# Kernel tuning notes

Measured on AMD Instinct MI355X. Metric: run time of the kernel, lower is better.

## Reference

```python
import jax, jax.numpy as jnp
import numpy as np

B, S, H, W, T, D = 256, 128, 14, 14, 12, 512


def _lin(key, fan_in, fan_out):
    k1, k2 = jax.random.split(key)
    bound = 1.0 / np.sqrt(fan_in)
    Wm = jax.random.uniform(k1, (fan_in, fan_out), jnp.float32, -bound, bound)
    b = jax.random.uniform(k2, (fan_out,), jnp.float32, -bound, bound)
    return Wm, b


def setup_inputs() -> dict:
    key = jax.random.key(0)
    ks = jax.random.split(key, 20)
    inp = {
        "ci_1": jax.random.normal(ks[0], (B, D), jnp.float32),
        "mi_1": jax.random.normal(ks[1], (B, D), jnp.float32),
        "q": jax.random.normal(ks[2], (B, D), jnp.float32),
        "cws": jax.random.normal(ks[3], (B, S, D), jnp.float32),
        "K": jax.random.normal(ks[4], (B, H, W, D), jnp.float32),
        "C_past": jax.random.normal(ks[5], (B, T, D), jnp.float32),
        "M_past": jax.random.normal(ks[6], (B, T, D), jnp.float32),
    }
    inp["W_cq"], inp["b_cq"] = _lin(ks[7], D, D)          # control_qi
    inp["W_cqi"], inp["b_cqi"] = _lin(ks[8], 2 * D, D)    # cqi_linear
    inp["W_cai"], inp["b_cai"] = _lin(ks[9], D, 1)        # cais_linear
    inp["W_rm"], inp["b_rm"] = _lin(ks[10], D, D)         # memory_read_m
    inp["W_rk"], inp["b_rk"] = _lin(ks[11], D, D)         # memory_read_k
    inp["W_rik"], inp["b_rik"] = _lin(ks[12], 2 * D, D)   # memory_read_ik
    inp["W_rci"], inp["b_rci"] = _lin(ks[13], D, D)       # memory_read_ci_i
    inp["W_wrm"], inp["b_wrm"] = _lin(ks[14], 2 * D, D)   # memory_write_ri_mi_1
    inp["W_wcc"], inp["b_wcc"] = _lin(ks[15], D, 1)       # memory_write_ci_cj
    inp["W_wsa"], inp["b_wsa"] = _lin(ks[16], D, D)       # memory_write_mi_sa
    inp["W_winfo"], inp["b_winfo"] = _lin(ks[17], D, D)   # memory_write_mi_info
    inp["W_wci"], inp["b_wci"] = _lin(ks[18], D, 1)       # memory_write_ci
    return inp


def reference(ci_1, mi_1, q, cws, K, C_past, M_past,
              W_cq, b_cq, W_cqi, b_cqi, W_cai, b_cai,
              W_rm, b_rm, W_rk, b_rk, W_rik, b_rik, W_rci, b_rci,
              W_wrm, b_wrm, W_wcc, b_wcc, W_wsa, b_wsa,
              W_winfo, b_winfo, W_wci, b_wci):
    # ---- control ----
    qi = q @ W_cq + b_cq                                        # [B,D]
    cqi = jnp.concatenate([ci_1, qi], axis=1) @ W_cqi + b_cqi   # [B,D]
    cqi_cws = cqi[:, None, :] * cws                             # [B,S,D]
    cai = cqi_cws @ W_cai + b_cai                               # [B,S,1]
    cvis = jax.nn.softmax(cai, axis=1)
    ci = (cvis * cws).sum(axis=1)                               # [B,D]

    # ---- read ----
    Ii = (mi_1 @ W_rm + b_rm)[:, None, None, :] * (K @ W_rk + b_rk)  # [B,H,W,D]
    Ii_prime = jnp.concatenate([Ii, K], axis=3) @ W_rik + b_rik      # [B,H,W,D]
    rai = (ci[:, None, None, :] * Ii_prime) @ W_rci + b_rci          # [B,H,W,D]
    rvi = jax.nn.softmax(rai, axis=1)   # softmax over H
    rvi = jax.nn.softmax(rvi, axis=2)   # then softmax of those probs over W (faithful)
    ri = (rvi * K).sum(axis=(1, 2))                                  # [B,D]

    # ---- write ----
    mi_info = jnp.concatenate([ri, mi_1], axis=1) @ W_wrm + b_wrm    # [B,D]
    ci_cj = ci[:, None, :] * C_past                                  # [B,T,D]
    saij = jax.nn.softmax(ci_cj @ W_wcc + b_wcc, axis=1)             # [B,T,1]
    mi_sa = (saij * M_past).sum(axis=1)                              # [B,D]
    mi_prime = (mi_sa @ W_wsa + b_wsa) + (mi_info @ W_winfo + b_winfo)
    gate = jax.nn.sigmoid(ci @ W_wci + b_wci)                        # [B,1]
    mi = gate * mi_1 + (1.0 - gate) * mi_prime
    return (ci, mi)
```

## Files before the change

### kernel.cpp

```cpp
#include <hip/hip_runtime.h>
#include <hip/hip_bf16.h>

typedef unsigned short u16;
typedef __attribute__((ext_vector_type(8))) short short8;
typedef __attribute__((ext_vector_type(4))) float f4;

static __device__ __forceinline__ float b2f(u16 u) {
    union { unsigned int i; float f; } x; x.i = ((unsigned int)u) << 16; return x.f;
}
static __device__ __forceinline__ u16 f2b(float f) {
    union { float f; unsigned int i; } x; x.f = f;
    unsigned int r = x.i + 0x7fffu + ((x.i >> 16) & 1u);
    return (u16)(r >> 16);
}
static __device__ __forceinline__ float wave_reduce_sum(float v) {
    #pragma unroll
    for (int off = 32; off > 0; off >>= 1) v += __shfl_down(v, off, 64);
    return v;
}
static __device__ __forceinline__ void gl2lds(const void* g, void* l) {
    __builtin_amdgcn_global_load_lds(
        (const __attribute__((address_space(1))) void*)g,
        (__attribute__((address_space(3))) void*)l, 16, 0, 0);
}

__global__ __launch_bounds__(256) void conv_f32_bf16(
    const float* __restrict__ src, u16* __restrict__ dst, int n)
{
    int i = (blockIdx.x * 256 + threadIdx.x) * 4;
    if (i >= n) return;
    float4 v = *(const float4*)(src + i);
    union { u16 u[4]; uint2 d; } o;
    o.u[0] = f2b(v.x); o.u[1] = f2b(v.y); o.u[2] = f2b(v.z); o.u[3] = f2b(v.w);
    *(uint2*)(dst + i) = o.d;
}

__global__ __launch_bounds__(256) void transpose_k(
    const float* __restrict__ in, u16* __restrict__ out,
    int K, int N, int out_stride, int k_off)
{
    __shared__ float t[32][33];
    int kb = blockIdx.x * 32, nb = blockIdx.y * 32;
    int tx = threadIdx.x, ty = threadIdx.y;
    #pragma unroll
    for (int i = 0; i < 4; i++)
        t[ty + i * 8][tx] = in[(size_t)(kb + ty + i * 8) * N + nb + tx];
    __syncthreads();
    #pragma unroll
    for (int i = 0; i < 4; i++)
        out[(size_t)(nb + ty + i * 8) * out_stride + k_off + kb + tx] =
            f2b(t[tx][ty + i * 8]);
}

template<int MT, int NT>
__global__ __launch_bounds__(256) void gemm_mfma(
    const u16* __restrict__ A0, const u16* __restrict__ A1,
    int M, int K0, int K1, int N,
    const u16* __restrict__ Bt,
    const float* __restrict__ bias0, const float* __restrict__ bias1,
    int epi_mode, const float* __restrict__ E, int m_div,
    const float* __restrict__ gate, const float* __restrict__ mi1,
    void* __restrict__ Cout, int out_f32)
{
    constexpr int BM = MT * 32, BN = NT * 32;
    constexpr int STG = (BM + BN) * 32;
    constexpr int NPF = MT / 2 + NT / 2;
    constexpr int STAGE_B = 3 * STG * 2;
    __shared__ __align__(16) char smem[STAGE_B];
    short* stg = (short*)smem;

    int tid  = threadIdx.x;
    int wave = tid >> 6, lane = tid & 63;
    int wm = wave >> 1, wn = wave & 1;
    int lrow = lane & 15, quad = lane >> 4;

    int gx = gridDim.x, gy = gridDim.y;
    int bx = blockIdx.x, by = blockIdx.y;
    if ((gy & 7) == 0) {
        int lin = by * gx + bx;
        int xcd = lin & 7, j = lin >> 3;
        by = xcd * (gy >> 3) + j / gx;
        bx = j % gx;
    }
    int bm0 = by * BM, bn0 = bx * BN;
    int Ktot = K0 + K1;
    int KT = Ktot >> 5;

    int r16 = lane >> 2, cc = lane & 3;
    int sw = (r16 >> 1) & 3;
    int coff = (cc ^ sw) * 8;

    auto stage = [&](int s, int k0) {
        const u16* asrc; int lda;
        if (k0 < K0) { asrc = A0 + k0; lda = K0; }
        else         { asrc = A1 + (k0 - K0); lda = K1; }
        short* As = stg + s * STG;
        short* Bs = As + BM * 32;
        #pragma unroll
        for (int i = 0; i < MT / 2; i++) {
            int ar = wave * (BM / 4) + 16 * i;
            gl2lds(asrc + (size_t)(bm0 + ar + r16) * lda + coff, As + ar * 32);
        }
        #pragma unroll
        for (int i = 0; i < NT / 2; i++) {
            int br = wave * (BN / 4) + 16 * i;
            gl2lds(Bt + (size_t)(bn0 + br + r16) * Ktot + k0 + coff, Bs + br * 32);
        }
    };

    f4 acc[MT][NT];
    #pragma unroll
    for (int i = 0; i < MT; i++)
        #pragma unroll
        for (int j = 0; j < NT; j++)
            acc[i][j] = (f4){0.f, 0.f, 0.f, 0.f};

    stage(0, 0);
    if (KT > 1) stage(1, 32);
    int sb = 0;
    int sw2 = (lrow >> 1) & 3;
    for (int kt = 0; kt < KT; kt++) {
        if (kt + 1 < KT) {
            if constexpr (NPF == 2)
                asm volatile("s_waitcnt vmcnt(2) lgkmcnt(0)\ns_barrier" ::: "memory");
            else
                asm volatile("s_waitcnt vmcnt(0) lgkmcnt(0)\ns_barrier" ::: "memory");
        } else {
            asm volatile("s_waitcnt vmcnt(0) lgkmcnt(0)\ns_barrier" ::: "memory");
        }
        const short* Ab = stg + sb * STG;
        const short* Bb = Ab + BM * 32;
        if (kt + 2 < KT) {
            int s2 = sb + 2; if (s2 >= 3) s2 -= 3;
            stage(s2, (kt + 2) * 32);
        }
        short8 af[MT], bfr[NT];
        #pragma unroll
        for (int mt = 0; mt < MT; mt++)
            af[mt] = *(const short8*)&Ab[(wm * (MT * 16) + mt * 16 + lrow) * 32 + (quad ^ sw2) * 8];
        #pragma unroll
        for (int nt = 0; nt < NT; nt++)
            bfr[nt] = *(const short8*)&Bb[(wn * (NT * 16) + nt * 16 + lrow) * 32 + (quad ^ sw2) * 8];
        #pragma unroll
        for (int mt = 0; mt < MT; mt++)
            #pragma unroll
            for (int nt = 0; nt < NT; nt++)
                acc[mt][nt] = __builtin_amdgcn_mfma_f32_16x16x32_bf16(
                    af[mt], bfr[nt], acc[mt][nt], 0, 0, 0);
        sb = (sb + 1 == 3) ? 0 : sb + 1;
    }

    #pragma unroll
    for (int nt = 0; nt < NT; nt++) {
        int n = bn0 + wn * (NT * 16) + nt * 16 + lrow;
        float bv = 0.f;
        if (bias0) bv += bias0[n];
        if (bias1) bv += bias1[n];
        #pragma unroll
        for (int mt = 0; mt < MT; mt++) {
            #pragma unroll
            for (int r = 0; r < 4; r++) {
                int m = bm0 + wm * (MT * 16) + mt * 16 + quad * 4 + r;
                float v = acc[mt][nt][r] + bv;
                if (epi_mode == 1) {
                    v *= E[(size_t)(m / m_div) * N + n];
                } else if (epi_mode == 2) {
                    float g = gate[m];
                    v = g * mi1[(size_t)m * N + n] + (1.f - g) * v;
                }
                if (out_f32) ((float*)Cout)[(size_t)m * N + n] = v;
                else         ((u16*)Cout)[(size_t)m * N + n] = f2b(v);
            }
        }
    }
}

__global__ __launch_bounds__(512, 2) void fused_read(
    const u16* __restrict__ kbf, int M,
    const u16* __restrict__ Wrk,  const float* __restrict__ brk,  const float* __restrict__ E1,
    const u16* __restrict__ Wrik, const float* __restrict__ brik, const float* __restrict__ E2,
    const u16* __restrict__ Wrci, const float* __restrict__ brci,
    u16* __restrict__ rai)
{
    __shared__ __align__(16) char smem[139264];
    short* g_tile = (short*)smem;
    short* stgbase = (short*)(smem + 65536);

    int tid = threadIdx.x, wave = tid >> 6, lane = tid & 63;
    int lrow = lane & 15, quad = lane >> 4;
    int r16 = lane >> 2, cc = lane & 3;
    int sw = (r16 >> 1) & 3;
    int coff = (cc ^ sw) * 8;
    int sw2 = (lrow >> 1) & 3;

    int bid = blockIdx.x;
    { int nb = gridDim.x; if ((nb & 7) == 0) { int x = bid & 7, j = bid >> 3; bid = x * (nb >> 3) + j; } }
    int bm0 = bid * 64;

    auto stageB = [&](short* bf, const u16* Wt, int ldk, int k0) {
        short* Bs = bf + 2048;
        #pragma unroll
        for (int i = 0; i < 4; i++) {
            int br = wave * 64 + i * 16;
            gl2lds(Wt + (size_t)(br + r16) * ldk + k0 + coff, Bs + br * 32);
        }
    };
    auto stageA = [&](short* bf, int k0) {
        if (wave < 4) {
            int ar = wave * 16;
            gl2lds(kbf + (size_t)(bm0 + ar + r16) * 512 + k0 + coff, bf + ar * 32);
        }
    };

    f4 acc[4][4];
    auto clr = [&]() {
        #pragma unroll
        for (int t = 0; t < 4; t++)
            #pragma unroll
            for (int nt = 0; nt < 4; nt++)
                acc[t][nt] = (f4){0.f, 0.f, 0.f, 0.f};
    };

    auto kstep = [&](const short* bf, int aMode, int kc0) {
        short8 af[4], bfrag[4];
        #pragma unroll
        for (int t = 0; t < 4; t++) {
            int R = t * 16 + lrow;
            if (aMode == 0)
                af[t] = *(const short8*)&bf[R * 32 + (quad ^ sw2) * 8];
            else {
                int kc = kc0 + quad;
                af[t] = *(const short8*)&g_tile[R * 512 + ((kc ^ (R & 7)) << 3)];
            }
        }
        const short* Bs = bf + 2048;
        #pragma unroll
        for (int nt = 0; nt < 4; nt++)
            bfrag[nt] = *(const short8*)&Bs[(wave * 64 + nt * 16 + lrow) * 32 + (quad ^ sw2) * 8];
        __builtin_amdgcn_s_setprio(1);
        #pragma unroll
        for (int t = 0; t < 4; t++)
            #pragma unroll
            for (int nt = 0; nt < 4; nt++)
                acc[t][nt] = __builtin_amdgcn_mfma_f32_16x16x32_bf16(
                    af[t], bfrag[nt], acc[t][nt], 0, 0, 0);
        __builtin_amdgcn_s_setprio(0);
    };

    int bt0 = bm0 / 196, bt1 = (bm0 + 63) / 196;
    int rsw = (bt1 != bt0) ? (bt1 * 196 - bm0) : 64;
    auto epi_to_gtile = [&](const float* bias, const float* E) {
        #pragma unroll
        for (int nt = 0; nt < 4; nt++) {
            int n = wave * 64 + nt * 16 + lrow;
            float bv = bias[n];
            float e0 = E[(size_t)bt0 * 512 + n];
            float e1 = E[(size_t)bt1 * 512 + n];
            #pragma unroll
            for (int t = 0; t < 4; t++)
                #pragma unroll
                for (int r = 0; r < 4; r++) {
                    int row = t * 16 + quad * 4 + r;
                    float e = (row < rsw) ? e0 : e1;
                    u16 h = f2b((acc[t][nt][r] + bv) * e);
                    int chunk = (n >> 3) ^ (row & 7);
                    g_tile[row * 512 + chunk * 8 + (n & 7)] = (short)h;
                }
        }
    };

    clr();
    stageA(stgbase, 0); stageB(stgbase, Wrk, 512, 0);
    for (int kt = 0; kt < 16; kt++) {
        short* cur = stgbase + (kt & 1) * 18432;
        short* nxt = stgbase + ((kt & 1) ^ 1) * 18432;
        if (kt + 1 < 16) {
            stageA(nxt, (kt + 1) * 32); stageB(nxt, Wrk, 512, (kt + 1) * 32);
            if (wave < 4) asm volatile("s_waitcnt vmcnt(5) lgkmcnt(0)\ns_barrier" ::: "memory");
            else          asm volatile("s_waitcnt vmcnt(4) lgkmcnt(0)\ns_barrier" ::: "memory");
        } else
            asm volatile("s_waitcnt vmcnt(0) lgkmcnt(0)\ns_barrier" ::: "memory");
        kstep(cur, 0, 0);
        asm volatile("s_waitcnt lgkmcnt(0)\ns_barrier" ::: "memory");
    }
    epi_to_gtile(brk, E1);
    __syncthreads();

    clr();
    stageB(stgbase, Wrik, 1024, 0);
    for (int kt = 0; kt < 16; kt++) {
        short* cur = stgbase + (kt & 1) * 18432;
        short* nxt = stgbase + ((kt & 1) ^ 1) * 18432;
        if (kt + 1 < 16) {
            stageB(nxt, Wrik, 1024, (kt + 1) * 32);
            asm volatile("s_waitcnt vmcnt(4) lgkmcnt(0)\ns_barrier" ::: "memory");
        } else
            asm volatile("s_waitcnt vmcnt(0) lgkmcnt(0)\ns_barrier" ::: "memory");
        kstep(cur, 1, kt * 4);
        asm volatile("s_waitcnt lgkmcnt(0)\ns_barrier" ::: "memory");
    }
    stageA(stgbase, 0); stageB(stgbase, Wrik, 1024, 512);
    for (int kt = 0; kt < 16; kt++) {
        short* cur = stgbase + (kt & 1) * 18432;
        short* nxt = stgbase + ((kt & 1) ^ 1) * 18432;
        if (kt + 1 < 16) {
            stageA(nxt, (kt + 1) * 32); stageB(nxt, Wrik, 1024, 512 + (kt + 1) * 32);
            if (wave < 4) asm volatile("s_waitcnt vmcnt(5) lgkmcnt(0)\ns_barrier" ::: "memory");
            else          asm volatile("s_waitcnt vmcnt(4) lgkmcnt(0)\ns_barrier" ::: "memory");
        } else
            asm volatile("s_waitcnt vmcnt(0) lgkmcnt(0)\ns_barrier" ::: "memory");
        kstep(cur, 0, 0);
        asm volatile("s_waitcnt lgkmcnt(0)\ns_barrier" ::: "memory");
    }
    epi_to_gtile(brik, E2);
    __syncthreads();

    clr();
    stageB(stgbase, Wrci, 512, 0);
    for (int kt = 0; kt < 16; kt++) {
        short* cur = stgbase + (kt & 1) * 18432;
        short* nxt = stgbase + ((kt & 1) ^ 1) * 18432;
        if (kt + 1 < 16) {
            stageB(nxt, Wrci, 512, (kt + 1) * 32);
            asm volatile("s_waitcnt vmcnt(4) lgkmcnt(0)\ns_barrier" ::: "memory");
        } else
            asm volatile("s_waitcnt vmcnt(0) lgkmcnt(0)\ns_barrier" ::: "memory");
        kstep(cur, 1, kt * 4);
        asm volatile("s_waitcnt lgkmcnt(0)\ns_barrier" ::: "memory");
    }
    #pragma unroll
    for (int nt = 0; nt < 4; nt++) {
        int n = wave * 64 + nt * 16 + lrow;
        float bv = brci[n];
        #pragma unroll
        for (int t = 0; t < 4; t++)
            #pragma unroll
            for (int r = 0; r < 4; r++) {
                int row = t * 16 + quad * 4 + r;
                g_tile[row * 512 + n] = (short)f2b(acc[t][nt][r] + bv);
            }
    }
    __syncthreads();
    #pragma unroll
    for (int p = 0; p < 8; p++) {
        int idx = p * 512 + tid;
        short8 v = *(const short8*)&g_tile[idx * 8];
        *(short8*)&rai[(size_t)bm0 * 512 + (size_t)idx * 8] = v;
    }
}

__global__ __launch_bounds__(256) void control_attn(
    const float* __restrict__ cqi, const float* __restrict__ cws,
    const float* __restrict__ Wcai, const float* __restrict__ bcai,
    float* __restrict__ ci_f32, float* __restrict__ ci_out)
{
    int b = blockIdx.x, tid = threadIdx.x;
    __shared__ float tW[512];
    __shared__ float p[128];
    __shared__ float inv_l;
    for (int d = tid; d < 512; d += 256)
        tW[d] = cqi[(size_t)b * 512 + d] * Wcai[d];
    __syncthreads();
    int wave = tid >> 6, lane = tid & 63;
    const float* cwsb = cws + (size_t)b * 128 * 512;
    for (int s = wave; s < 128; s += 4) {
        const float* row = cwsb + (size_t)s * 512 + lane * 8;
        float acc = 0.f;
        #pragma unroll
        for (int j = 0; j < 8; j++) acc += tW[lane * 8 + j] * row[j];
        acc = wave_reduce_sum(acc);
        if (lane == 0) p[s] = acc + bcai[0];
    }
    __syncthreads();
    if (tid == 0) {
        float m = -1e30f;
        for (int s = 0; s < 128; s++) m = fmaxf(m, p[s]);
        float l = 0.f;
        for (int s = 0; s < 128; s++) { float e = __expf(p[s] - m); p[s] = e; l += e; }
        inv_l = 1.f / l;
    }
    __syncthreads();
    float inv = inv_l;
    for (int d = tid; d < 512; d += 256) {
        float acc = 0.f;
        for (int s = 0; s < 128; s++) acc += p[s] * cwsb[(size_t)s * 512 + d];
        acc *= inv;
        ci_f32[(size_t)b * 512 + d] = acc;
        ci_out[(size_t)b * 512 + d] = acc;
    }
}

__global__ __launch_bounds__(256) void read_reduce(
    const u16* __restrict__ rai, const u16* __restrict__ Kb, u16* __restrict__ ri)
{
    int b = blockIdx.x >> 1;
    int d = ((blockIdx.x & 1) << 8) + threadIdx.x;
    const u16* rb = rai + (size_t)b * 196 * 512 + d;
    const u16* kb = Kb + (size_t)b * 196 * 512 + d;
    float m1[14], il1[14];
    #pragma unroll
    for (int w = 0; w < 14; w++) {
        float m = -1e30f, s = 0.f;
        #pragma unroll
        for (int h = 0; h < 14; h++) {
            float v = b2f(rb[(size_t)(h * 14 + w) * 512]);
            float nm = fmaxf(m, v);
            s = s * __expf(m - nm) + __expf(v - nm);
            m = nm;
        }
        m1[w] = m; il1[w] = 1.f / s;
    }
    float acc = 0.f;
    #pragma unroll
    for (int h = 0; h < 14; h++) {
        float pv[14], ss = 0.f;
        #pragma unroll
        for (int w = 0; w < 14; w++) {
            float pr = __expf(b2f(rb[(size_t)(h * 14 + w) * 512]) - m1[w]) * il1[w];
            float e = __expf(pr);
            pv[w] = e; ss += e;
        }
        float il2 = 1.f / ss;
        #pragma unroll
        for (int w = 0; w < 14; w++)
            acc += pv[w] * il2 * b2f(kb[(size_t)(h * 14 + w) * 512]);
    }
    ri[(size_t)b * 512 + d] = f2b(acc);
}

__global__ __launch_bounds__(256) void write_attn(
    const float* __restrict__ ci_f32, const float* __restrict__ C_past,
    const float* __restrict__ M_past,
    const float* __restrict__ Wwcc, const float* __restrict__ bwcc,
    const float* __restrict__ Wwci, const float* __restrict__ bwci,
    u16* __restrict__ mi_sa, float* __restrict__ gate)
{
    int b = blockIdx.x, tid = threadIdx.x;
    __shared__ float c[512];
    __shared__ float pt[12];
    __shared__ float red[256];
    for (int d = tid; d < 512; d += 256) c[d] = ci_f32[(size_t)b * 512 + d];
    __syncthreads();
    float g = 0.f;
    for (int d = tid; d < 512; d += 256) g += c[d] * Wwci[d];
    red[tid] = g;
    __syncthreads();
    for (int s = 128; s > 0; s >>= 1) {
        if (tid < s) red[tid] += red[tid + s];
        __syncthreads();
    }
    int wave = tid >> 6, lane = tid & 63;
    const float* cp = C_past + (size_t)b * 12 * 512;
    for (int t = wave; t < 12; t += 4) {
        float acc = 0.f;
        #pragma unroll
        for (int j = 0; j < 8; j++) {
            int d = lane * 8 + j;
            acc += c[d] * Wwcc[d] * cp[(size_t)t * 512 + d];
        }
        acc = wave_reduce_sum(acc);
        if (lane == 0) pt[t] = acc + bwcc[0];
    }
    __syncthreads();
    if (tid == 0) {
        float m = -1e30f;
        for (int t = 0; t < 12; t++) m = fmaxf(m, pt[t]);
        float l = 0.f;
        for (int t = 0; t < 12; t++) { float e = __expf(pt[t] - m); pt[t] = e; l += e; }
        float invl = 1.f / l;
        for (int t = 0; t < 12; t++) pt[t] *= invl;
        gate[b] = 1.f / (1.f + __expf(-(red[0] + bwci[0])));
    }
    __syncthreads();
    const float* mp = M_past + (size_t)b * 12 * 512;
    for (int d = tid; d < 512; d += 256) {
        float acc = 0.f;
        #pragma unroll
        for (int t = 0; t < 12; t++) acc += pt[t] * mp[(size_t)t * 512 + d];
        mi_sa[(size_t)b * 512 + d] = f2b(acc);
    }
}

extern "C" void kernel_launch(void* const* d_in, const int* in_sizes, int n_in,
                              void* d_out, int out_size, void* d_ws, size_t ws_size,
                              hipStream_t stream) {
    (void)in_sizes; (void)n_in; (void)out_size;
    const int B = 256, D = 512, HW = 196;

    const float* ci_1   = (const float*)d_in[0];
    const float* mi_1   = (const float*)d_in[1];
    const float* q      = (const float*)d_in[2];
    const float* cws    = (const float*)d_in[3];
    const float* Kin    = (const float*)d_in[4];
    const float* C_past = (const float*)d_in[5];
    const float* M_past = (const float*)d_in[6];
    const float* W_cq   = (const float*)d_in[7];
    const float* b_cq   = (const float*)d_in[8];
    const float* W_cqi  = (const float*)d_in[9];
    const float* b_cqi  = (const float*)d_in[10];
    const float* W_cai  = (const float*)d_in[11];
    const float* b_cai  = (const float*)d_in[12];
    const float* W_rm   = (const float*)d_in[13];
    const float* b_rm   = (const float*)d_in[14];
    const float* W_rk   = (const float*)d_in[15];
    const float* b_rk   = (const float*)d_in[16];
    const float* W_rik  = (const float*)d_in[17];
    const float* b_rik  = (const float*)d_in[18];
    const float* W_rci  = (const float*)d_in[19];
    const float* b_rci  = (const float*)d_in[20];
    const float* W_wrm  = (const float*)d_in[21];
    const float* b_wrm  = (const float*)d_in[22];
    const float* W_wcc  = (const float*)d_in[23];
    const float* b_wcc  = (const float*)d_in[24];
    const float* W_wsa  = (const float*)d_in[25];
    const float* b_wsa  = (const float*)d_in[26];
    const float* W_winfo= (const float*)d_in[27];
    const float* b_winfo= (const float*)d_in[28];
    const float* W_wci  = (const float*)d_in[29];
    const float* b_wci  = (const float*)d_in[30];

    float* out_ci = (float*)d_out;
    float* out_mi = (float*)d_out + (size_t)B * D;

    char* ws = (char*)d_ws;
    size_t off = 0;
    auto alloc = [&](size_t bytes) -> void* {
        void* p = ws + off; off += (bytes + 255) & ~(size_t)255; return p;
    };
    u16* wt_cq    = (u16*)alloc((size_t)D * D * 2);
    u16* wt_cqi   = (u16*)alloc((size_t)D * 2 * D * 2);
    u16* wt_rm    = (u16*)alloc((size_t)D * D * 2);
    u16* wt_rk    = (u16*)alloc((size_t)D * D * 2);
    u16* wt_rik   = (u16*)alloc((size_t)D * 2 * D * 2);
    u16* wt_rci   = (u16*)alloc((size_t)D * D * 2);
    u16* wt_wrm   = (u16*)alloc((size_t)D * 2 * D * 2);
    u16* wt_wsi   = (u16*)alloc((size_t)D * 2 * D * 2);
    u16* qb       = (u16*)alloc((size_t)B * D * 2);
    u16* cib      = (u16*)alloc((size_t)B * D * 2);
    u16* mib      = (u16*)alloc((size_t)B * D * 2);
    u16* qi_buf   = (u16*)alloc((size_t)B * D * 2);
    float* cqi_f32= (float*)alloc((size_t)B * D * 4);
    float* rm_f32 = (float*)alloc((size_t)B * D * 4);
    float* ci_f32 = (float*)alloc((size_t)B * D * 4);
    u16* ri_buf   = (u16*)alloc((size_t)B * D * 2);
    u16* misa_buf = (u16*)alloc((size_t)B * D * 2);
    u16* minfo_buf= (u16*)alloc((size_t)B * D * 2);
    float* gate_b = (float*)alloc((size_t)B * 4);

    int chunk_b = 256;
    while (chunk_b > 32) {
        size_t need = off + 2 * (((size_t)chunk_b * HW * D * 2 + 255) & ~(size_t)255);
        if (need <= ws_size) break;
        chunk_b >>= 1;
    }
    u16* kbf  = (u16*)alloc((size_t)chunk_b * HW * D * 2);
    u16* big1 = (u16*)alloc((size_t)chunk_b * HW * D * 2);

    dim3 tb(32, 8);
    transpose_k<<<dim3(D / 32, D / 32), tb, 0, stream>>>(W_cq,   wt_cq,  D,     D, D,     0);
    transpose_k<<<dim3(2 * D / 32, D / 32), tb, 0, stream>>>(W_cqi, wt_cqi, 2 * D, D, 2 * D, 0);
    transpose_k<<<dim3(D / 32, D / 32), tb, 0, stream>>>(W_rm,   wt_rm,  D,     D, D,     0);
    transpose_k<<<dim3(D / 32, D / 32), tb, 0, stream>>>(W_rk,   wt_rk,  D,     D, D,     0);
    transpose_k<<<dim3(2 * D / 32, D / 32), tb, 0, stream>>>(W_rik, wt_rik, 2 * D, D, 2 * D, 0);
    transpose_k<<<dim3(D / 32, D / 32), tb, 0, stream>>>(W_rci,  wt_rci, D,     D, D,     0);
    transpose_k<<<dim3(2 * D / 32, D / 32), tb, 0, stream>>>(W_wrm, wt_wrm, 2 * D, D, 2 * D, 0);
    transpose_k<<<dim3(D / 32, D / 32), tb, 0, stream>>>(W_wsa,  wt_wsi, D,     D, 2 * D, 0);
    transpose_k<<<dim3(D / 32, D / 32), tb, 0, stream>>>(W_winfo,wt_wsi, D,     D, 2 * D, D);

    int nbd = B * D;
    conv_f32_bf16<<<nbd / 1024, 256, 0, stream>>>(q, qb, nbd);
    conv_f32_bf16<<<nbd / 1024, 256, 0, stream>>>(ci_1, cib, nbd);
    conv_f32_bf16<<<nbd / 1024, 256, 0, stream>>>(mi_1, mib, nbd);

    dim3 gsmall(D / 64, B / 64);

    gemm_mfma<2,2><<<gsmall, 256, 0, stream>>>(qb, nullptr, B, D, 0, D, wt_cq, b_cq, nullptr,
                                               0, nullptr, 1, nullptr, nullptr, qi_buf, 0);
    gemm_mfma<2,2><<<gsmall, 256, 0, stream>>>(cib, qi_buf, B, D, D, D, wt_cqi, b_cqi, nullptr,
                                               0, nullptr, 1, nullptr, nullptr, cqi_f32, 1);
    control_attn<<<B, 256, 0, stream>>>(cqi_f32, cws, W_cai, b_cai, ci_f32, out_ci);
    gemm_mfma<2,2><<<gsmall, 256, 0, stream>>>(mib, nullptr, B, D, 0, D, wt_rm, b_rm, nullptr,
                                               0, nullptr, 1, nullptr, nullptr, rm_f32, 1);

    for (int c = 0; c < B; c += chunk_b) {
        int mrows = chunk_b * HW;
        const float* Kc = Kin + (size_t)c * HW * D;
        conv_f32_bf16<<<(mrows * D) / 1024, 256, 0, stream>>>(Kc, kbf, mrows * D);
        fused_read<<<mrows / 64, 512, 0, stream>>>(
            kbf, mrows,
            wt_rk,  b_rk,  rm_f32 + (size_t)c * D,
            wt_rik, b_rik, ci_f32 + (size_t)c * D,
            wt_rci, b_rci,
            big1);
        read_reduce<<<chunk_b * 2, 256, 0, stream>>>(big1, kbf, ri_buf + (size_t)c * D);
    }

    gemm_mfma<2,2><<<gsmall, 256, 0, stream>>>(ri_buf, mib, B, D, D, D, wt_wrm, b_wrm, nullptr,
                                               0, nullptr, 1, nullptr, nullptr, minfo_buf, 0);
    write_attn<<<B, 256, 0, stream>>>(ci_f32, C_past, M_past, W_wcc, b_wcc, W_wci, b_wci,
                                      misa_buf, gate_b);
    gemm_mfma<2,2><<<gsmall, 256, 0, stream>>>(misa_buf, minfo_buf, B, D, D, D, wt_wsi,
                                               b_wsa, b_winfo, 2, nullptr, 1, gate_b, mi_1,
                                               out_mi, 1);
}
```

Before: 600.9 us.

## Run fused_read with 16 waves per block and batch weight-prep launches

fused_read now uses 1024 threads arranged as a 2x8 wave grid. Each wave computes a 32x64 output tile instead of 64x64, which halves the accumulator registers per wave and splits the B-tile staging across more waves, with the vmcnt waits adjusted to match. The aim is more waves in flight to hide LDS and global-load latency in the dominant kernel. The risk is that the tighter launch bound on registers causes spills, and that the larger block adds barrier cost. Separately, the nine weight transposes are merged into one batched launch and the three activation conversions into one, to cut launch overhead.

New measurement: 591.5 us. Within noise of the previous version (-1.6%).

```diff
diff --git a/kernel.cpp b/kernel.cpp
--- a/kernel.cpp
+++ b/kernel.cpp
@@ -35,12 +35,41 @@
     *(uint2*)(dst + i) = o.d;
 }
 
-__global__ __launch_bounds__(256) void transpose_k(
-    const float* __restrict__ in, u16* __restrict__ out,
-    int K, int N, int out_stride, int k_off)
+__global__ __launch_bounds__(256) void conv3_f32_bf16(
+    const float* __restrict__ s0, const float* __restrict__ s1, const float* __restrict__ s2,
+    u16* __restrict__ d0, u16* __restrict__ d1, u16* __restrict__ d2)
+{
+    int which = blockIdx.x >> 7;
+    int i = ((blockIdx.x & 127) * 256 + threadIdx.x) * 4;
+    const float* s = (which == 0) ? s0 : (which == 1) ? s1 : s2;
+    u16* d = (which == 0) ? d0 : (which == 1) ? d1 : d2;
+    float4 v = *(const float4*)(s + i);
+    union { u16 u[4]; uint2 d; } o;
+    o.u[0] = f2b(v.x); o.u[1] = f2b(v.y); o.u[2] = f2b(v.z); o.u[3] = f2b(v.w);
+    *(uint2*)(d + i) = o.d;
+}
+
+struct TBatch {
+    const float* in[9];
+    u16* out[9];
+    int K[9];
+    int ostride[9];
+    int koff[9];
+    int tbase[9];
+};
+
+__global__ __launch_bounds__(256) void transpose_batch(TBatch a)
 {
     __shared__ float t[32][33];
-    int kb = blockIdx.x * 32, nb = blockIdx.y * 32;
+    int b = blockIdx.x;
+    int w = 0;
+    #pragma unroll
+    for (int i = 1; i < 9; i++) if (b >= a.tbase[i]) w = i;
+    int lt = b - a.tbase[w];
+    int kb = (lt >> 4) * 32, nb = (lt & 15) * 32;
+    const float* in = a.in[w];
+    u16* out = a.out[w];
+    int N = 512, ostride = a.ostride[w], koff = a.koff[w];
     int tx = threadIdx.x, ty = threadIdx.y;
     #pragma unroll
     for (int i = 0; i < 4; i++)
@@ -48,7 +77,7 @@
     __syncthreads();
     #pragma unroll
     for (int i = 0; i < 4; i++)
-        out[(size_t)(nb + ty + i * 8) * out_stride + k_off + kb + tx] =
+        out[(size_t)(nb + ty + i * 8) * ostride + koff + kb + tx] =
             f2b(t[tx][ty + i * 8]);
 }
 
@@ -175,7 +204,7 @@
     }
 }
 
-__global__ __launch_bounds__(512, 2) void fused_read(
+__global__ __launch_bounds__(1024, 4) void fused_read(
     const u16* __restrict__ kbf, int M,
     const u16* __restrict__ Wrk,  const float* __restrict__ brk,  const float* __restrict__ E1,
     const u16* __restrict__ Wrik, const float* __restrict__ brik, const float* __restrict__ E2,
@@ -187,6 +216,7 @@
     short* stgbase = (short*)(smem + 65536);
 
     int tid = threadIdx.x, wave = tid >> 6, lane = tid & 63;
+    int wr = wave >> 3, wc = wave & 7;
     int lrow = lane & 15, quad = lane >> 4;
     int r16 = lane >> 2, cc = lane & 3;
     int sw = (r16 >> 1) & 3;
@@ -200,8 +230,8 @@
     auto stageB = [&](short* bf, const u16* Wt, int ldk, int k0) {
         short* Bs = bf + 2048;
         #pragma unroll
-        for (int i = 0; i < 4; i++) {
-            int br = wave * 64 + i * 16;
+        for (int i = 0; i < 2; i++) {
+            int br = wave * 32 + i * 16;
             gl2lds(Wt + (size_t)(br + r16) * ldk + k0 + coff, Bs + br * 32);
         }
     };
@@ -212,20 +242,20 @@
         }
     };
 
-    f4 acc[4][4];
+    f4 acc[2][4];
     auto clr = [&]() {
         #pragma unroll
-        for (int t = 0; t < 4; t++)
+        for (int t = 0; t < 2; t++)
             #pragma unroll
             for (int nt = 0; nt < 4; nt++)
                 acc[t][nt] = (f4){0.f, 0.f, 0.f, 0.f};
     };
 
     auto kstep = [&](const short* bf, int aMode, int kc0) {
-        short8 af[4], bfrag[4];
-        #pragma unroll
-        for (int t = 0; t < 4; t++) {
-            int R = t * 16 + lrow;
+        short8 af[2], bfrag[4];
+        #pragma unroll
+        for (int t = 0; t < 2; t++) {
+            int R = wr * 32 + t * 16 + lrow;
             if (aMode == 0)
                 af[t] = *(const short8*)&bf[R * 32 + (quad ^ sw2) * 8];
             else {
@@ -236,10 +266,10 @@
         const short* Bs = bf + 2048;
         #pragma unroll
         for (int nt = 0; nt < 4; nt++)
-            bfrag[nt] = *(const short8*)&Bs[(wave * 64 + nt * 16 + lrow) * 32 + (quad ^ sw2) * 8];
+            bfrag[nt] = *(const short8*)&Bs[(wc * 64 + nt * 16 + lrow) * 32 + (quad ^ sw2) * 8];
         __builtin_amdgcn_s_setprio(1);
         #pragma unroll
-        for (int t = 0; t < 4; t++)
+        for (int t = 0; t < 2; t++)
             #pragma unroll
             for (int nt = 0; nt < 4; nt++)
                 acc[t][nt] = __builtin_amdgcn_mfma_f32_16x16x32_bf16(
@@ -252,15 +282,15 @@
     auto epi_to_gtile = [&](const float* bias, const float* E) {
         #pragma unroll
         for (int nt = 0; nt < 4; nt++) {
-            int n = wave * 64 + nt * 16 + lrow;
+            int n = wc * 64 + nt * 16 + lrow;
             float bv = bias[n];
             float e0 = E[(size_t)bt0 * 512 + n];
             float e1 = E[(size_t)bt1 * 512 + n];
             #pragma unroll
-            for (int t = 0; t < 4; t++)
+            for (int t = 0; t < 2; t++)
                 #pragma unroll
                 for (int r = 0; r < 4; r++) {
-                    int row = t * 16 + quad * 4 + r;
+                    int row = wr * 32 + t * 16 + quad * 4 + r;
                     float e = (row < rsw) ? e0 : e1;
                     u16 h = f2b((acc[t][nt][r] + bv) * e);
                     int chunk = (n >> 3) ^ (row & 7);
@@ -276,8 +306,8 @@
         short* nxt = stgbase + ((kt & 1) ^ 1) * 18432;
         if (kt + 1 < 16) {
             stageA(nxt, (kt + 1) * 32); stageB(nxt, Wrk, 512, (kt + 1) * 32);
-            if (wave < 4) asm volatile("s_waitcnt vmcnt(5) lgkmcnt(0)\ns_barrier" ::: "memory");
-            else          asm volatile("s_waitcnt vmcnt(4) lgkmcnt(0)\ns_barrier" ::: "memory");
+            if (wave < 4) asm volatile("s_waitcnt vmcnt(3) lgkmcnt(0)\ns_barrier" ::: "memory");
+            else          asm volatile("s_waitcnt vmcnt(2) lgkmcnt(0)\ns_barrier" ::: "memory");
         } else
             asm volatile("s_waitcnt vmcnt(0) lgkmcnt(0)\ns_barrier" ::: "memory");
         kstep(cur, 0, 0);
@@ -293,7 +323,7 @@
         short* nxt = stgbase + ((kt & 1) ^ 1) * 18432;
         if (kt + 1 < 16) {
             stageB(nxt, Wrik, 1024, (kt + 1) * 32);
-            asm volatile("s_waitcnt vmcnt(4) lgkmcnt(0)\ns_barrier" ::: "memory");
+            asm volatile("s_waitcnt vmcnt(2) lgkmcnt(0)\ns_barrier" ::: "memory");
         } else
             asm volatile("s_waitcnt vmcnt(0) lgkmcnt(0)\ns_barrier" ::: "memory");
         kstep(cur, 1, kt * 4);
@@ -305,8 +335,8 @@
         short* nxt = stgbase + ((kt & 1) ^ 1) * 18432;
         if (kt + 1 < 16) {
             stageA(nxt, (kt + 1) * 32); stageB(nxt, Wrik, 1024, 512 + (kt + 1) * 32);
-            if (wave < 4) asm volatile("s_waitcnt vmcnt(5) lgkmcnt(0)\ns_barrier" ::: "memory");
-            else          asm volatile("s_waitcnt vmcnt(4) lgkmcnt(0)\ns_barrier" ::: "memory");
+            if (wave < 4) asm volatile("s_waitcnt vmcnt(3) lgkmcnt(0)\ns_barrier" ::: "memory");
+            else          asm volatile("s_waitcnt vmcnt(2) lgkmcnt(0)\ns_barrier" ::: "memory");
         } else
             asm volatile("s_waitcnt vmcnt(0) lgkmcnt(0)\ns_barrier" ::: "memory");
         kstep(cur, 0, 0);
@@ -322,7 +352,7 @@
         short* nxt = stgbase + ((kt & 1) ^ 1) * 18432;
         if (kt + 1 < 16) {
             stageB(nxt, Wrci, 512, (kt + 1) * 32);
-            asm volatile("s_waitcnt vmcnt(4) lgkmcnt(0)\ns_barrier" ::: "memory");
+            asm volatile("s_waitcnt vmcnt(2) lgkmcnt(0)\ns_barrier" ::: "memory");
         } else
             asm volatile("s_waitcnt vmcnt(0) lgkmcnt(0)\ns_barrier" ::: "memory");
         kstep(cur, 1, kt * 4);
@@ -330,20 +360,20 @@
     }
     #pragma unroll
     for (int nt = 0; nt < 4; nt++) {
-        int n = wave * 64 + nt * 16 + lrow;
+        int n = wc * 64 + nt * 16 + lrow;
         float bv = brci[n];
         #pragma unroll
-        for (int t = 0; t < 4; t++)
+        for (int t = 0; t < 2; t++)
             #pragma unroll
             for (int r = 0; r < 4; r++) {
-                int row = t * 16 + quad * 4 + r;
+                int row = wr * 32 + t * 16 + quad * 4 + r;
                 g_tile[row * 512 + n] = (short)f2b(acc[t][nt][r] + bv);
             }
     }
     __syncthreads();
     #pragma unroll
-    for (int p = 0; p < 8; p++) {
-        int idx = p * 512 + tid;
+    for (int p = 0; p < 4; p++) {
+        int idx = p * 1024 + tid;
         short8 v = *(const short8*)&g_tile[idx * 8];
         *(short8*)&rai[(size_t)bm0 * 512 + (size_t)idx * 8] = v;
     }
@@ -556,21 +586,21 @@
     u16* kbf  = (u16*)alloc((size_t)chunk_b * HW * D * 2);
     u16* big1 = (u16*)alloc((size_t)chunk_b * HW * D * 2);
 
-    dim3 tb(32, 8);
-    transpose_k<<<dim3(D / 32, D / 32), tb, 0, stream>>>(W_cq,   wt_cq,  D,     D, D,     0);
-    transpose_k<<<dim3(2 * D / 32, D / 32), tb, 0, stream>>>(W_cqi, wt_cqi, 2 * D, D, 2 * D, 0);
-    transpose_k<<<dim3(D / 32, D / 32), tb, 0, stream>>>(W_rm,   wt_rm,  D,     D, D,     0);
-    transpose_k<<<dim3(D / 32, D / 32), tb, 0, stream>>>(W_rk,   wt_rk,  D,     D, D,     0);
-    transpose_k<<<dim3(2 * D / 32, D / 32), tb, 0, stream>>>(W_rik, wt_rik, 2 * D, D, 2 * D, 0);
-    transpose_k<<<dim3(D / 32, D / 32), tb, 0, stream>>>(W_rci,  wt_rci, D,     D, D,     0);
-    transpose_k<<<dim3(2 * D / 32, D / 32), tb, 0, stream>>>(W_wrm, wt_wrm, 2 * D, D, 2 * D, 0);
-    transpose_k<<<dim3(D / 32, D / 32), tb, 0, stream>>>(W_wsa,  wt_wsi, D,     D, 2 * D, 0);
-    transpose_k<<<dim3(D / 32, D / 32), tb, 0, stream>>>(W_winfo,wt_wsi, D,     D, 2 * D, D);
-
-    int nbd = B * D;
-    conv_f32_bf16<<<nbd / 1024, 256, 0, stream>>>(q, qb, nbd);
-    conv_f32_bf16<<<nbd / 1024, 256, 0, stream>>>(ci_1, cib, nbd);
-    conv_f32_bf16<<<nbd / 1024, 256, 0, stream>>>(mi_1, mib, nbd);
+    TBatch tb;
+    const float* tin[9] = {W_cq, W_cqi, W_rm, W_rk, W_rik, W_rci, W_wrm, W_wsa, W_winfo};
+    u16* tout[9] = {wt_cq, wt_cqi, wt_rm, wt_rk, wt_rik, wt_rci, wt_wrm, wt_wsi, wt_wsi};
+    int tK[9]  = {512, 1024, 512, 512, 1024, 512, 1024, 512, 512};
+    int tos[9] = {512, 1024, 512, 512, 1024, 512, 1024, 1024, 1024};
+    int tko[9] = {0, 0, 0, 0, 0, 0, 0, 0, 512};
+    int tbase = 0;
+    for (int i = 0; i < 9; i++) {
+        tb.in[i] = tin[i]; tb.out[i] = tout[i]; tb.K[i] = tK[i];
+        tb.ostride[i] = tos[i]; tb.koff[i] = tko[i]; tb.tbase[i] = tbase;
+        tbase += (tK[i] / 32) * 16;
+    }
+    transpose_batch<<<tbase, dim3(32, 8), 0, stream>>>(tb);
+
+    conv3_f32_bf16<<<384, 256, 0, stream>>>(q, ci_1, mi_1, qb, cib, mib);
 
     dim3 gsmall(D / 64, B / 64);
 
@@ -586,7 +616,7 @@
         int mrows = chunk_b * HW;
         const float* Kc = Kin + (size_t)c * HW * D;
         conv_f32_bf16<<<(mrows * D) / 1024, 256, 0, stream>>>(Kc, kbf, mrows * D);
-        fused_read<<<mrows / 64, 512, 0, stream>>>(
+        fused_read<<<mrows / 64, 1024, 0, stream>>>(
             kbf, mrows,
             wt_rk,  b_rk,  rm_f32 + (size_t)c * D,
             wt_rik, b_rik, ci_f32 + (size_t)c * D,
```
